# Kernel tuning notes

Hardware: AMD Instinct MI355X
Metric: run time of the kernel (lower is better)

Reference implementation:

```python
import jax, jax.numpy as jnp
import numpy as np

B, D, H, C = 512, 1024, 512, 4


def setup_inputs() -> dict:
    key = jax.random.key(0)
    k_x, k_v, k_w = jax.random.split(key, 3)
    # x holds categorical values in [0, C) used as float multipliers
    x = jax.random.randint(k_x, (B, D), 0, C).astype(jnp.float32)
    # xavier_normal_ per torch fan computation: V fan_in=D*C, fan_out=H*C; W fan_in=D, fan_out=H
    V = jax.random.normal(k_v, (H, D, C), jnp.float32) * np.float32(np.sqrt(2.0 / (D * C + H * C)))
    b = jnp.zeros((D, C), jnp.float32)
    W = jax.random.normal(k_w, (H, D), jnp.float32) * np.float32(np.sqrt(2.0 / (D + H)))
    c = jnp.zeros((1, H), jnp.float32)
    return {"x": x, "V": V, "b": b, "W": W, "c": c}


def _nade_forward(x, V, b, W, c):
    Bsz = x.shape[0]
    a0 = jnp.broadcast_to(c, (Bsz, c.shape[1]))  # [B, H]
    # per-step slices stacked along leading D axis for lax.scan
    xs = (jnp.transpose(V, (1, 0, 2)),  # [D, H, C]
          b,                            # [D, C]
          W.T,                          # [D, H]
          x.T)                          # [D, B]

    def step(a, inp):
        V_d, b_d, w_d, x_d = inp
        h = jax.nn.sigmoid(a)                 # [B, H]
        logits = h @ V_d + b_d                # [B, C]
        p = jax.nn.log_softmax(logits, axis=1)
        a_new = a + x_d[:, None] * w_d[None, :]  # rank-1 update of running preactivation
        return a_new, (logits, p)

    _, (logits, p) = jax.lax.scan(step, a0, xs)   # each [D, B, C]
    y_hat = jnp.transpose(logits, (1, 0, 2)).reshape(Bsz, -1)  # [B, D*C], d-major blocks of size C
    p_hat = jnp.transpose(p, (1, 0, 2)).reshape(Bsz, -1)
    return y_hat, p_hat


def reference(x, V, b, W, c):
    return _nade_forward(x, V, b, W, c)
```

## Files before the change

kernel.cpp:

```cpp
#include <hip/hip_runtime.h>


#define Bv 512
#define Dv 1024
#define Hv 512
#define Cv 4
#define Kv 32
#define DCv 32

#define L2E 1.4426950408889634f
#define LN2 0.6931471805599453f

typedef __attribute__((ext_vector_type(8))) short short8;
typedef __attribute__((ext_vector_type(4))) float f32x4;

__device__ __forceinline__ float fexp2(float x) { return __builtin_amdgcn_exp2f(x); }
__device__ __forceinline__ float flog2(float x) { return __builtin_amdgcn_logf(x); }
__device__ __forceinline__ float frcp(float x)  { return __builtin_amdgcn_rcpf(x); }

__device__ __forceinline__ unsigned bf16pk(float lo, float hi) {
    return __builtin_amdgcn_perm(__float_as_uint(hi), __float_as_uint(lo), 0x07060302u);
}
__device__ __forceinline__ unsigned short bf16rne(float f) {
    unsigned u = __float_as_uint(f);
    return (unsigned short)((u + 0x7FFFu + ((u >> 16) & 1u)) >> 16);
}

__global__ __launch_bounds__(256) void k_prep(const float* __restrict__ W,
                                              const float* __restrict__ x,
                                              float* __restrict__ WtL,
                                              float* __restrict__ xt) {
    __shared__ float t[64][65];
    const int mb   = blockIdx.x >> 7;
    const int tile = blockIdx.x & 127;
    const int tr   = tile >> 4;
    const int tc   = tile & 15;
    const float* src = mb ? x : W;
    float* dst       = mb ? xt : WtL;
    const float scale = mb ? 1.0f : L2E;
    const int lx = threadIdx.x & 15;
    const int ly = threadIdx.x >> 4;

#pragma unroll
    for (int r = 0; r < 64; r += 16) {
        int row = r + ly;
        float4 v = *(const float4*)(src + (size_t)(tr * 64 + row) * Dv + tc * 64 + lx * 4);
        t[row][lx * 4 + 0] = v.x;
        t[row][lx * 4 + 1] = v.y;
        t[row][lx * 4 + 2] = v.z;
        t[row][lx * 4 + 3] = v.w;
    }
    __syncthreads();
#pragma unroll
    for (int r = 0; r < 64; r += 16) {
        int row = r + ly;
        float4 o = make_float4(t[lx * 4 + 0][row] * scale,
                               t[lx * 4 + 1][row] * scale,
                               t[lx * 4 + 2][row] * scale,
                               t[lx * 4 + 3][row] * scale);
        *(float4*)(dst + (size_t)(tc * 64 + row) * 512 + tr * 64 + lx * 4) = o;
    }
}

__global__ __launch_bounds__(256) void k_prepv(const float* __restrict__ V,
                                               unsigned short* __restrict__ VtA4) {
    __shared__ unsigned short tile[4 * 16 * 16 * 8];
    const int d0 = blockIdx.x * 4;
    const int dd = threadIdx.x & 3;
    const int hb0 = threadIdx.x >> 2;
#pragma unroll
    for (int p = 0; p < 8; ++p) {
        int h = p * 64 + hb0;
        float4 v = *(const float4*)(V + ((size_t)h * Dv + d0 + dd) * Cv);
        int hb = h >> 5, q = (h >> 3) & 3, j = h & 7;
        int base = ((dd * 16 + hb) * 16 + q * 4) * 8 + j;
        tile[base + 0 * 8] = bf16rne(v.x);
        tile[base + 1 * 8] = bf16rne(v.y);
        tile[base + 2 * 8] = bf16rne(v.z);
        tile[base + 3 * 8] = bf16rne(v.w);
    }
    __syncthreads();
    uint4* dst = (uint4*)(VtA4 + (size_t)d0 * 2048);
    const uint4* src = (const uint4*)tile;
    for (int tt = threadIdx.x; tt < 1024; tt += 256) dst[tt] = src[tt];
}

__global__ __launch_bounds__(512) void k_partial(const float* __restrict__ x,
                          const float* __restrict__ WtL, float* __restrict__ A0) {
    int k  = blockIdx.x >> 6;
    int bg = blockIdx.x & 63;
    int h  = threadIdx.x;
    int d0 = k * DCv;

    __shared__ float xs[DCv * 8];
    if (threadIdx.x < DCv * 8) {
        int g = threadIdx.x >> 5;
        int j = threadIdx.x & 31;
        xs[j * 8 + g] = x[(size_t)(bg * 8 + g) * Dv + d0 + j];
    }
    __syncthreads();

    float acc[8];
#pragma unroll
    for (int g = 0; g < 8; ++g) acc[g] = 0.0f;

    const float* wp = WtL + (size_t)d0 * Hv + h;
    for (int j = 0; j < DCv; ++j) {
        float wv = wp[(size_t)j * Hv];
        const float4 x0 = *(const float4*)(xs + j * 8);
        const float4 x1 = *(const float4*)(xs + j * 8 + 4);
        acc[0] = fmaf(x0.x, wv, acc[0]);
        acc[1] = fmaf(x0.y, wv, acc[1]);
        acc[2] = fmaf(x0.z, wv, acc[2]);
        acc[3] = fmaf(x0.w, wv, acc[3]);
        acc[4] = fmaf(x1.x, wv, acc[4]);
        acc[5] = fmaf(x1.y, wv, acc[5]);
        acc[6] = fmaf(x1.z, wv, acc[6]);
        acc[7] = fmaf(x1.w, wv, acc[7]);
    }
#pragma unroll
    for (int g = 0; g < 8; ++g)
        A0[((size_t)k * Bv + bg * 8 + g) * Hv + h] = acc[g];
}

__global__ void k_prefix(float* __restrict__ A0, const float* __restrict__ cbias) {
    int gid = blockIdx.x * blockDim.x + threadIdx.x;
    int h = gid & (Hv - 1);
    int bi = gid >> 9;
    float run = cbias[h] * L2E;
    float* p = A0 + (size_t)bi * Hv + h;
    for (int k = 0; k < Kv; ++k) {
        float t = p[(size_t)k * Bv * Hv];
        p[(size_t)k * Bv * Hv] = run;
        run += t;
    }
}

__global__ __launch_bounds__(256, 4) void k_main(
        const float* __restrict__ xt, const float* __restrict__ bbias,
        const unsigned short* __restrict__ VtA4, const float* __restrict__ WtL,
        const float* __restrict__ A0, float* __restrict__ out) {
    const int k    = blockIdx.x >> 5;
    const int bg   = blockIdx.x & 31;
    const int wid  = threadIdx.x >> 6;
    const int lane = threadIdx.x & 63;
    const int bl   = lane & 15;
    const int quad = lane >> 4;
    const int b    = bg * 16 + bl;
    const int d0   = k * DCv;
    const int stp  = wid >> 1;
    const bool isP = wid & 1;

    __shared__ f32x4 red[2][2][4][64];

    float a[32];
    {
        const float* ap = A0 + ((size_t)k * Bv + b) * Hv + wid * 128 + quad * 8;
#pragma unroll
        for (int kb = 0; kb < 4; ++kb) {
            float4 t0 = *(const float4*)(ap + kb * 32);
            float4 t1 = *(const float4*)(ap + kb * 32 + 4);
            a[kb*8+0]=t0.x; a[kb*8+1]=t0.y; a[kb*8+2]=t0.z; a[kb*8+3]=t0.w;
            a[kb*8+4]=t1.x; a[kb*8+5]=t1.y; a[kb*8+6]=t1.z; a[kb*8+7]=t1.w;
        }
    }

    const bool act = (bl < 4);
    const unsigned short* vp = VtA4 + (((size_t)d0 * 16 + wid * 4) * 16 + quad * 4 + bl) * 8;
    const float* wp = WtL + (size_t)d0 * Hv + wid * 128 + quad * 8;
    const float* xp = xt + (size_t)d0 * Bv + b;
    const float* bp = bbias + (d0 + stp) * Cv;
    float* sp = out + (isP ? (size_t)Bv * Dv * Cv : (size_t)0)
                    + (size_t)b * Dv * Cv + (d0 + stp) * Cv;

    const short8 zfrag = {0,0,0,0,0,0,0,0};

    for (int i1 = 0; i1 < DCv / 2; ++i1) {
        short8 afA[4], afB[4];
#pragma unroll
        for (int kb = 0; kb < 4; ++kb)
            afA[kb] = act ? *(const short8*)(vp + kb * 128) : zfrag;
#pragma unroll
        for (int kb = 0; kb < 4; ++kb)
            afB[kb] = act ? *(const short8*)(vp + 2048 + kb * 128) : zfrag;
        float xdA = xp[0];
        float xdB = xp[Bv];
        float4 bbv = *(const float4*)bp;

        unsigned pkA[16];
#pragma unroll
        for (int m = 0; m < 32; m += 2) {
            float s0 = frcp(1.0f + fexp2(-a[m]));
            float s1 = frcp(1.0f + fexp2(-a[m + 1]));
            pkA[m >> 1] = bf16pk(s0, s1);
        }
        f32x4 accA = {0.f, 0.f, 0.f, 0.f};
#pragma unroll
        for (int kb = 0; kb < 4; ++kb) {
            union { unsigned u[4]; short8 s; } cv;
            cv.u[0] = pkA[kb*4+0]; cv.u[1] = pkA[kb*4+1];
            cv.u[2] = pkA[kb*4+2]; cv.u[3] = pkA[kb*4+3];
            accA = __builtin_amdgcn_mfma_f32_16x16x32_bf16(afA[kb], cv.s, accA, 0, 0, 0);
        }
#pragma unroll
        for (int kb = 0; kb < 4; ++kb)
#pragma unroll
            for (int j = 0; j < 8; ++j)
                a[kb*8+j] = fmaf(xdA, wp[kb*32+j], a[kb*8+j]);

        unsigned pkB[16];
#pragma unroll
        for (int m = 0; m < 32; m += 2) {
            float s0 = frcp(1.0f + fexp2(-a[m]));
            float s1 = frcp(1.0f + fexp2(-a[m + 1]));
            pkB[m >> 1] = bf16pk(s0, s1);
        }
        f32x4 accB = {0.f, 0.f, 0.f, 0.f};
#pragma unroll
        for (int kb = 0; kb < 4; ++kb) {
            union { unsigned u[4]; short8 s; } cv;
            cv.u[0] = pkB[kb*4+0]; cv.u[1] = pkB[kb*4+1];
            cv.u[2] = pkB[kb*4+2]; cv.u[3] = pkB[kb*4+3];
            accB = __builtin_amdgcn_mfma_f32_16x16x32_bf16(afB[kb], cv.s, accB, 0, 0, 0);
        }
#pragma unroll
        for (int kb = 0; kb < 4; ++kb)
#pragma unroll
            for (int j = 0; j < 8; ++j)
                a[kb*8+j] = fmaf(xdB, wp[Hv + kb*32+j], a[kb*8+j]);

        red[i1 & 1][0][wid][lane] = accA;
        red[i1 & 1][1][wid][lane] = accB;
        __syncthreads();

        f32x4 r0 = red[i1 & 1][stp][0][lane];
        f32x4 r1 = red[i1 & 1][stp][1][lane];
        f32x4 r2 = red[i1 & 1][stp][2][lane];
        f32x4 r3 = red[i1 & 1][stp][3][lane];
        float w0 = r0.x + r1.x + r2.x + r3.x + bbv.x;
        float w1 = r0.y + r1.y + r2.y + r3.y + bbv.y;
        float w2 = r0.z + r1.z + r2.z + r3.z + bbv.z;
        float w3 = r0.w + r1.w + r2.w + r3.w + bbv.w;

        if (!isP) {
            if (quad == 0) *(float4*)sp = make_float4(w0, w1, w2, w3);
        } else {
            float mx = fmaxf(fmaxf(w0, w1), fmaxf(w2, w3));
            float e0 = fexp2((w0 - mx) * L2E);
            float e1 = fexp2((w1 - mx) * L2E);
            float e2 = fexp2((w2 - mx) * L2E);
            float e3 = fexp2((w3 - mx) * L2E);
            float lse = mx + flog2(e0 + e1 + e2 + e3) * LN2;
            if (quad == 0)
                *(float4*)sp = make_float4(w0 - lse, w1 - lse, w2 - lse, w3 - lse);
        }

        vp += 2 * 2048;
        wp += 2 * Hv;
        xp += 2 * Bv;
        bp += 2 * Cv;
        sp += 2 * Cv;
    }
}

extern "C" void kernel_launch(void* const* d_in, const int* in_sizes, int n_in,
                              void* d_out, int out_size, void* d_ws, size_t ws_size,
                              hipStream_t stream) {
    const float* x  = (const float*)d_in[0];
    const float* V  = (const float*)d_in[1];
    const float* bb = (const float*)d_in[2];
    const float* W  = (const float*)d_in[3];
    const float* cb = (const float*)d_in[4];
    float* out = (float*)d_out;

    char* ws = (char*)d_ws;
    unsigned short* VtA4 = (unsigned short*)ws;
    float* WtL = (float*)(ws + (size_t)4 * 1024 * 1024);
    float* xt  = (float*)(ws + (size_t)6 * 1024 * 1024);
    float* A0  = (float*)(ws + (size_t)8 * 1024 * 1024);

    k_prep<<<256, 256, 0, stream>>>(W, x, WtL, xt);
    k_prepv<<<Dv / 4, 256, 0, stream>>>(V, VtA4);
    k_partial<<<Kv * (Bv / 8), 512, 0, stream>>>(x, WtL, A0);
    k_prefix<<<(Bv * Hv) / 256, 256, 0, stream>>>(A0, cb);
    k_main<<<Kv * 32, 256, 0, stream>>>(xt, bb, VtA4, WtL, A0, out);
}
```

Measured before the change: 170.3 us.

## Merge independent prep kernels into one launch and prefetch next-step operands in main loop

Splits the W transpose into its own small kernel. The V bf16 repack, the x transpose and the partial A0 computation now run as branches of one 512-thread kernel, which removes launches and lets the independent work share the GPU. In the main loop, the V fragments, x values and bias for the next step are loaded before the reduction barrier, so their latency overlaps the sync and softmax. This adds register pressure in k_main, which may lower occupancy, and the last prefetch reads one step past the end of the V and x arrays.

New measurement: 213.7 us. 25.5% more time.

```diff
diff --git a/kernel.cpp b/kernel.cpp
--- a/kernel.cpp
+++ b/kernel.cpp
@@ -26,25 +26,18 @@
     return (unsigned short)((u + 0x7FFFu + ((u >> 16) & 1u)) >> 16);
 }
 
-__global__ __launch_bounds__(256) void k_prep(const float* __restrict__ W,
-                                              const float* __restrict__ x,
-                                              float* __restrict__ WtL,
-                                              float* __restrict__ xt) {
+__global__ __launch_bounds__(256) void k_prepW(const float* __restrict__ W,
+                                               float* __restrict__ WtL) {
     __shared__ float t[64][65];
-    const int mb   = blockIdx.x >> 7;
-    const int tile = blockIdx.x & 127;
+    const int tile = blockIdx.x;
     const int tr   = tile >> 4;
     const int tc   = tile & 15;
-    const float* src = mb ? x : W;
-    float* dst       = mb ? xt : WtL;
-    const float scale = mb ? 1.0f : L2E;
     const int lx = threadIdx.x & 15;
     const int ly = threadIdx.x >> 4;
-
 #pragma unroll
     for (int r = 0; r < 64; r += 16) {
         int row = r + ly;
-        float4 v = *(const float4*)(src + (size_t)(tr * 64 + row) * Dv + tc * 64 + lx * 4);
+        float4 v = *(const float4*)(W + (size_t)(tr * 64 + row) * Dv + tc * 64 + lx * 4);
         t[row][lx * 4 + 0] = v.x;
         t[row][lx * 4 + 1] = v.y;
         t[row][lx * 4 + 2] = v.z;
@@ -54,73 +47,101 @@
 #pragma unroll
     for (int r = 0; r < 64; r += 16) {
         int row = r + ly;
-        float4 o = make_float4(t[lx * 4 + 0][row] * scale,
-                               t[lx * 4 + 1][row] * scale,
-                               t[lx * 4 + 2][row] * scale,
-                               t[lx * 4 + 3][row] * scale);
-        *(float4*)(dst + (size_t)(tc * 64 + row) * 512 + tr * 64 + lx * 4) = o;
-    }
-}
-
-__global__ __launch_bounds__(256) void k_prepv(const float* __restrict__ V,
-                                               unsigned short* __restrict__ VtA4) {
-    __shared__ unsigned short tile[4 * 16 * 16 * 8];
-    const int d0 = blockIdx.x * 4;
-    const int dd = threadIdx.x & 3;
-    const int hb0 = threadIdx.x >> 2;
-#pragma unroll
-    for (int p = 0; p < 8; ++p) {
-        int h = p * 64 + hb0;
-        float4 v = *(const float4*)(V + ((size_t)h * Dv + d0 + dd) * Cv);
-        int hb = h >> 5, q = (h >> 3) & 3, j = h & 7;
-        int base = ((dd * 16 + hb) * 16 + q * 4) * 8 + j;
-        tile[base + 0 * 8] = bf16rne(v.x);
-        tile[base + 1 * 8] = bf16rne(v.y);
-        tile[base + 2 * 8] = bf16rne(v.z);
-        tile[base + 3 * 8] = bf16rne(v.w);
-    }
-    __syncthreads();
-    uint4* dst = (uint4*)(VtA4 + (size_t)d0 * 2048);
-    const uint4* src = (const uint4*)tile;
-    for (int tt = threadIdx.x; tt < 1024; tt += 256) dst[tt] = src[tt];
-}
-
-__global__ __launch_bounds__(512) void k_partial(const float* __restrict__ x,
-                          const float* __restrict__ WtL, float* __restrict__ A0) {
-    int k  = blockIdx.x >> 6;
-    int bg = blockIdx.x & 63;
-    int h  = threadIdx.x;
-    int d0 = k * DCv;
-
-    __shared__ float xs[DCv * 8];
-    if (threadIdx.x < DCv * 8) {
-        int g = threadIdx.x >> 5;
-        int j = threadIdx.x & 31;
-        xs[j * 8 + g] = x[(size_t)(bg * 8 + g) * Dv + d0 + j];
-    }
-    __syncthreads();
-
-    float acc[8];
-#pragma unroll
-    for (int g = 0; g < 8; ++g) acc[g] = 0.0f;
-
-    const float* wp = WtL + (size_t)d0 * Hv + h;
-    for (int j = 0; j < DCv; ++j) {
-        float wv = wp[(size_t)j * Hv];
-        const float4 x0 = *(const float4*)(xs + j * 8);
-        const float4 x1 = *(const float4*)(xs + j * 8 + 4);
-        acc[0] = fmaf(x0.x, wv, acc[0]);
-        acc[1] = fmaf(x0.y, wv, acc[1]);
-        acc[2] = fmaf(x0.z, wv, acc[2]);
-        acc[3] = fmaf(x0.w, wv, acc[3]);
-        acc[4] = fmaf(x1.x, wv, acc[4]);
-        acc[5] = fmaf(x1.y, wv, acc[5]);
-        acc[6] = fmaf(x1.z, wv, acc[6]);
-        acc[7] = fmaf(x1.w, wv, acc[7]);
-    }
-#pragma unroll
-    for (int g = 0; g < 8; ++g)
-        A0[((size_t)k * Bv + bg * 8 + g) * Hv + h] = acc[g];
+        float4 o = make_float4(t[lx * 4 + 0][row] * L2E,
+                               t[lx * 4 + 1][row] * L2E,
+                               t[lx * 4 + 2][row] * L2E,
+                               t[lx * 4 + 3][row] * L2E);
+        *(float4*)(WtL + (size_t)(tc * 64 + row) * 512 + tr * 64 + lx * 4) = o;
+    }
+}
+
+__global__ __launch_bounds__(512) void k_mid(
+        const float* __restrict__ x, const float* __restrict__ V,
+        const float* __restrict__ WtL,
+        unsigned short* __restrict__ VtA4, float* __restrict__ xt,
+        float* __restrict__ A0) {
+    __shared__ __align__(16) char smem[16640];
+    const int blk = blockIdx.x;
+
+    if (blk < 2048) {
+        float* xs = (float*)smem;
+        const int k  = blk >> 6;
+        const int bg = blk & 63;
+        const int h  = threadIdx.x;
+        const int d0 = k * DCv;
+        if (threadIdx.x < DCv * 8) {
+            int g = threadIdx.x >> 5;
+            int j = threadIdx.x & 31;
+            xs[j * 8 + g] = x[(size_t)(bg * 8 + g) * Dv + d0 + j];
+        }
+        __syncthreads();
+        float acc[8];
+#pragma unroll
+        for (int g = 0; g < 8; ++g) acc[g] = 0.0f;
+        const float* wp = WtL + (size_t)d0 * Hv + h;
+        for (int j = 0; j < DCv; ++j) {
+            float wv = wp[(size_t)j * Hv];
+            const float4 x0 = *(const float4*)(xs + j * 8);
+            const float4 x1 = *(const float4*)(xs + j * 8 + 4);
+            acc[0] = fmaf(x0.x, wv, acc[0]);
+            acc[1] = fmaf(x0.y, wv, acc[1]);
+            acc[2] = fmaf(x0.z, wv, acc[2]);
+            acc[3] = fmaf(x0.w, wv, acc[3]);
+            acc[4] = fmaf(x1.x, wv, acc[4]);
+            acc[5] = fmaf(x1.y, wv, acc[5]);
+            acc[6] = fmaf(x1.z, wv, acc[6]);
+            acc[7] = fmaf(x1.w, wv, acc[7]);
+        }
+#pragma unroll
+        for (int g = 0; g < 8; ++g)
+            A0[((size_t)k * Bv + bg * 8 + g) * Hv + h] = acc[g];
+    } else if (blk < 2304) {
+        unsigned short* tile = (unsigned short*)smem;
+        const int d0  = (blk - 2048) * 4;
+        const int dd  = threadIdx.x & 3;
+        const int hb0 = threadIdx.x >> 2;
+#pragma unroll
+        for (int p = 0; p < 4; ++p) {
+            int h = p * 128 + hb0;
+            float4 v = *(const float4*)(V + ((size_t)h * Dv + d0 + dd) * Cv);
+            int hb = h >> 5, q = (h >> 3) & 3, j = h & 7;
+            int base = ((dd * 16 + hb) * 16 + q * 4) * 8 + j;
+            tile[base + 0 * 8] = bf16rne(v.x);
+            tile[base + 1 * 8] = bf16rne(v.y);
+            tile[base + 2 * 8] = bf16rne(v.z);
+            tile[base + 3 * 8] = bf16rne(v.w);
+        }
+        __syncthreads();
+        uint4* dst = (uint4*)(VtA4 + (size_t)d0 * 2048);
+        const uint4* srcp = (const uint4*)tile;
+        for (int tt = threadIdx.x; tt < 1024; tt += 512) dst[tt] = srcp[tt];
+    } else {
+        float (*t)[65] = (float(*)[65])smem;
+        const int tile = blk - 2304;
+        const int tr   = tile >> 4;
+        const int tc   = tile & 15;
+        const int lx = threadIdx.x & 15;
+        const int ly = threadIdx.x >> 4;
+#pragma unroll
+        for (int r = 0; r < 64; r += 32) {
+            int row = r + ly;
+            float4 v = *(const float4*)(x + (size_t)(tr * 64 + row) * Dv + tc * 64 + lx * 4);
+            t[row][lx * 4 + 0] = v.x;
+            t[row][lx * 4 + 1] = v.y;
+            t[row][lx * 4 + 2] = v.z;
+            t[row][lx * 4 + 3] = v.w;
+        }
+        __syncthreads();
+#pragma unroll
+        for (int r = 0; r < 64; r += 32) {
+            int row = r + ly;
+            float4 o = make_float4(t[lx * 4 + 0][row],
+                                   t[lx * 4 + 1][row],
+                                   t[lx * 4 + 2][row],
+                                   t[lx * 4 + 3][row]);
+            *(float4*)(xt + (size_t)(tc * 64 + row) * 512 + tr * 64 + lx * 4) = o;
+        }
+    }
 }
 
 __global__ void k_prefix(float* __restrict__ A0, const float* __restrict__ cbias) {
@@ -175,18 +196,18 @@
 
     const short8 zfrag = {0,0,0,0,0,0,0,0};
 
+    short8 afA[4], afB[4];
+#pragma unroll
+    for (int kb = 0; kb < 4; ++kb)
+        afA[kb] = act ? *(const short8*)(vp + kb * 128) : zfrag;
+#pragma unroll
+    for (int kb = 0; kb < 4; ++kb)
+        afB[kb] = act ? *(const short8*)(vp + 2048 + kb * 128) : zfrag;
+    float xdA = xp[0];
+    float xdB = xp[Bv];
+    float4 bbv = *(const float4*)bp;
+
     for (int i1 = 0; i1 < DCv / 2; ++i1) {
-        short8 afA[4], afB[4];
-#pragma unroll
-        for (int kb = 0; kb < 4; ++kb)
-            afA[kb] = act ? *(const short8*)(vp + kb * 128) : zfrag;
-#pragma unroll
-        for (int kb = 0; kb < 4; ++kb)
-            afB[kb] = act ? *(const short8*)(vp + 2048 + kb * 128) : zfrag;
-        float xdA = xp[0];
-        float xdB = xp[Bv];
-        float4 bbv = *(const float4*)bp;
-
         unsigned pkA[16];
 #pragma unroll
         for (int m = 0; m < 32; m += 2) {
@@ -229,14 +250,29 @@
             for (int j = 0; j < 8; ++j)
                 a[kb*8+j] = fmaf(xdB, wp[Hv + kb*32+j], a[kb*8+j]);
 
-        red[i1 & 1][0][wid][lane] = accA;
-        red[i1 & 1][1][wid][lane] = accB;
+        const unsigned short* vpn = vp + 2 * 2048;
+        const float* xpn = xp + 2 * Bv;
+        const float* bpn = (i1 < DCv / 2 - 1) ? (bp + 2 * Cv) : bp;
+        short8 nfA[4], nfB[4];
+#pragma unroll
+        for (int kb = 0; kb < 4; ++kb)
+            nfA[kb] = act ? *(const short8*)(vpn + kb * 128) : zfrag;
+#pragma unroll
+        for (int kb = 0; kb < 4; ++kb)
+            nfB[kb] = act ? *(const short8*)(vpn + 2048 + kb * 128) : zfrag;
+        float nxA = xpn[0];
+        float nxB = xpn[Bv];
+        float4 nbb = *(const float4*)bpn;
+
+        const int buf = i1 & 1;
+        red[buf][0][wid][lane] = accA;
+        red[buf][1][wid][lane] = accB;
         __syncthreads();
 
-        f32x4 r0 = red[i1 & 1][stp][0][lane];
-        f32x4 r1 = red[i1 & 1][stp][1][lane];
-        f32x4 r2 = red[i1 & 1][stp][2][lane];
-        f32x4 r3 = red[i1 & 1][stp][3][lane];
+        f32x4 r0 = red[buf][stp][0][lane];
+        f32x4 r1 = red[buf][stp][1][lane];
+        f32x4 r2 = red[buf][stp][2][lane];
+        f32x4 r3 = red[buf][stp][3][lane];
         float w0 = r0.x + r1.x + r2.x + r3.x + bbv.x;
         float w1 = r0.y + r1.y + r2.y + r3.y + bbv.y;
         float w2 = r0.z + r1.z + r2.z + r3.z + bbv.z;
@@ -255,10 +291,11 @@
                 *(float4*)sp = make_float4(w0 - lse, w1 - lse, w2 - lse, w3 - lse);
         }
 
-        vp += 2 * 2048;
+#pragma unroll
+        for (int kb = 0; kb < 4; ++kb) { afA[kb] = nfA[kb]; afB[kb] = nfB[kb]; }
+        xdA = nxA; xdB = nxB; bbv = nbb;
+        vp = vpn; xp = xpn; bp = bpn;
         wp += 2 * Hv;
-        xp += 2 * Bv;
-        bp += 2 * Cv;
         sp += 2 * Cv;
     }
 }
@@ -279,9 +316,8 @@
     float* xt  = (float*)(ws + (size_t)6 * 1024 * 1024);
     float* A0  = (float*)(ws + (size_t)8 * 1024 * 1024);
 
-    k_prep<<<256, 256, 0, stream>>>(W, x, WtL, xt);
-    k_prepv<<<Dv / 4, 256, 0, stream>>>(V, VtA4);
-    k_partial<<<Kv * (Bv / 8), 512, 0, stream>>>(x, WtL, A0);
+    k_prepW<<<128, 256, 0, stream>>>(W, WtL);
+    k_mid<<<2432, 512, 0, stream>>>(x, V, WtL, VtA4, xt, A0);
     k_prefix<<<(Bv * Hv) / 256, 256, 0, stream>>>(A0, cb);
     k_main<<<Kv * 32, 256, 0, stream>>>(xt, bb, VtA4, WtL, A0, out);
 }
```
